# Optimization experiments

Measured on AMD Instinct MI355X. Metric: run time of the kernel, lower is better.

Reference implementation:

```python
import jax, jax.numpy as jnp
import numpy as np

B, S, ENC, DEC = 32, 2048, 1024, 1024
NEG = -1e9


def setup_inputs() -> dict:
    key = jax.random.key(0)
    k1, k2, k3, k4, k5, k6 = jax.random.split(key, 6)
    scale = lambda d: 1.0 / np.sqrt(d)
    return {
        "enc_outputs": jax.random.normal(k1, (B, S, ENC), jnp.float32),
        "dec_hidden": jax.random.normal(k2, (B, DEC), jnp.float32),
        "mask": jax.random.randint(k3, (B, S), 0, 2, jnp.int32),
        "W": jax.random.normal(k4, (ENC, DEC), jnp.float32) * scale(ENC),
        "U": jax.random.normal(k5, (DEC, DEC), jnp.float32) * scale(DEC),
        "v": jax.random.normal(k6, (DEC,), jnp.float32) * scale(DEC),
    }


def reference(enc_outputs, dec_hidden, mask, W, U, v):
    # scores: [B,S] = tanh(enc W + dec U) . v
    proj = jnp.tanh(jnp.einsum('bse,ed->bsd', enc_outputs, W)
                    + jnp.einsum('be,ed->bd', dec_hidden, U)[:, None, :])
    scores = jnp.einsum('bsd,d->bs', proj, v)
    scores = jnp.where(mask == 0, NEG, scores)
    attn = jax.nn.softmax(scores, axis=-1)
    context = jnp.einsum('bs,bse->be', attn, enc_outputs)
    return context, attn
```

## Files before the change

### kernel.cpp

```cpp
#include <hip/hip_runtime.h>
#include <hip/hip_bf16.h>
#include <stdint.h>

#define B_    32
#define S_    2048
#define ENC_  1024
#define DEC_  1024
#define M_    (B_*S_)

typedef __attribute__((ext_vector_type(8))) short bf16x8;
typedef __attribute__((ext_vector_type(4))) float f32x4;

__device__ __forceinline__ unsigned short f2bf(float f) {
  unsigned u = __builtin_bit_cast(unsigned, f);
  u += 0x7FFFu + ((u >> 16) & 1u);
  return (unsigned short)(u >> 16);
}
__device__ __forceinline__ float bf2f(unsigned short u) {
  unsigned x = ((unsigned)u) << 16;
  return __builtin_bit_cast(float, x);
}
__device__ __forceinline__ void async_copy16(void* lds_dst, const void* g_src) {
  __builtin_amdgcn_global_load_lds(
      (const __attribute__((address_space(1))) void*)g_src,
      (__attribute__((address_space(3))) void*)lds_dst, 16, 0, 0);
}
__device__ __forceinline__ float tanh_fast(float x) {
  return 1.f - 2.f / (__expf(2.f * x) + 1.f);
}

__global__ __launch_bounds__(256) void prep_kernel(
    const float* __restrict__ enc, unsigned short* __restrict__ enc16,
    const float* __restrict__ W, const float* __restrict__ dec,
    const float* __restrict__ U, unsigned short* __restrict__ Wt,
    float* __restrict__ t_buf, float* __restrict__ scoresZ,
    float* __restrict__ ctxZ) {
  __shared__ float smem[32 * 33];
  const int blk = blockIdx.x, tid = threadIdx.x;
  if (blk < 8192) {
    const float4* in = (const float4*)enc;
    ushort4* out = (ushort4*)enc16;
    #pragma unroll
    for (int i = 0; i < 8; ++i) {
      int idx = blk * 2048 + i * 256 + tid;
      float4 f = in[idx];
      ushort4 o;
      o.x = f2bf(f.x); o.y = f2bf(f.y); o.z = f2bf(f.z); o.w = f2bf(f.w);
      out[idx] = o;
    }
  } else if (blk < 9216) {
    const int q = blk - 8192;
    const int e0 = (q & 31) * 32, d0 = (q >> 5) * 32;
    const int tx = tid & 31, ty = tid >> 5;
    #pragma unroll
    for (int i = 0; i < 4; ++i)
      smem[(ty + i*8)*33 + tx] = W[(size_t)(e0 + ty + i*8) * DEC_ + d0 + tx];
    __syncthreads();
    #pragma unroll
    for (int i = 0; i < 4; ++i)
      Wt[(size_t)(d0 + ty + i*8) * ENC_ + e0 + tx] = f2bf(smem[tx*33 + ty + i*8]);
  } else if (blk < 9472) {
    const int q = blk - 9216;
    const int dblk = q & 7, b = q >> 3;
    const int d = dblk * 128 + (tid & 127);
    const int h = tid >> 7;
    float acc = 0.f;
    const float* dv = dec + b * DEC_ + h * 512;
    const float* Uc = U + (size_t)(h * 512) * DEC_ + d;
    for (int e = 0; e < 512; ++e) acc += dv[e] * Uc[(size_t)e * DEC_];
    smem[tid] = acc;
    __syncthreads();
    if (tid < 128) t_buf[b * DEC_ + d] = smem[tid] + smem[tid + 128];
  } else {
    const int q = blk - 9472;
    float4 z = {0.f, 0.f, 0.f, 0.f};
    for (int i = tid; i < 512; i += 256) ((float4*)scoresZ)[q * 512 + i] = z;
    for (int i = tid; i < 256; i += 256) ((float4*)ctxZ)[q * 256 + i] = z;
  }
}


#define WT_L  asm volatile("s_waitcnt lgkmcnt(0)" ::: "memory")
#define WT_V4 asm volatile("s_waitcnt vmcnt(4) lgkmcnt(0)" ::: "memory")
#define WT_V0 asm volatile("s_waitcnt vmcnt(0) lgkmcnt(0)" ::: "memory")

#define PHASE(CBUF, Q, KK, BLOAD, TAILWAIT, ...) do {                       \
    bf16x8 af_[4];                                                          \
    const int aA_ = (KK ? aAddr1 : aAddr0) + (CBUF)*32768 + (Q)*16384;      \
    _Pragma("unroll")                                                       \
    for (int mi = 0; mi < 4; ++mi)                                          \
      af_[mi] = *(const bf16x8*)(lds + aA_ + mi*2048);                      \
    if (BLOAD) {                                                            \
      const int bA_ = (KK ? bAddr1 : bAddr0) + (CBUF)*32768;                \
      _Pragma("unroll")                                                     \
      for (int ni = 0; ni < 4; ++ni)                                        \
        bfr[KK][ni] = *(const bf16x8*)(lds + bA_ + ni*2048);                \
    }                                                                       \
    __VA_ARGS__;                                                            \
    __builtin_amdgcn_s_barrier();                                           \
    __builtin_amdgcn_sched_barrier(0);                                      \
    __builtin_amdgcn_s_setprio(1);                                          \
    _Pragma("unroll")                                                       \
    for (int mi = 0; mi < 4; ++mi) {                                        \
      _Pragma("unroll")                                                     \
      for (int ni = 0; ni < 4; ++ni)                                        \
        acc[(Q)*4+mi][ni] = __builtin_amdgcn_mfma_f32_16x16x32_bf16(        \
            af_[mi], bfr[KK][ni], acc[(Q)*4+mi][ni], 0, 0, 0);              \
    }                                                                       \
    __builtin_amdgcn_s_setprio(0);                                          \
    __builtin_amdgcn_sched_barrier(0);                                      \
    TAILWAIT;                                                               \
    __builtin_amdgcn_s_barrier();                                           \
  } while (0)

__global__ __launch_bounds__(512, 2) void scores_kernel(
    const unsigned short* __restrict__ A,
    const unsigned short* __restrict__ Bt,
    const float* __restrict__ tb,
    const float* __restrict__ v,
    float* __restrict__ scores)
{
  extern __shared__ char lds[];

  const int tid  = threadIdx.x;
  const int lane = tid & 63;
  const int wid  = tid >> 6;
  const int wr = wid >> 2, wc = wid & 3;
  const int fr = lane & 15, fq = lane >> 4;

  const int bid = blockIdx.x;
  const int logical = (bid & 7) * 128 + (bid >> 3);
  const int m_blk = logical >> 2, n_blk = logical & 3;
  const int m0 = m_blk << 8;
  const int n0 = n_blk << 8;
  const int b  = m_blk >> 3;

  const int srow   = tid >> 3;
  const int kchunk = (((tid & 7) ^ (srow & 7)) << 3);
  const unsigned short* aP0 = A  + (size_t)(m0       + srow) * ENC_ + kchunk;
  const unsigned short* aP1 = A  + (size_t)(m0 + 64  + srow) * ENC_ + kchunk;
  const unsigned short* aP2 = A  + (size_t)(m0 + 128 + srow) * ENC_ + kchunk;
  const unsigned short* aP3 = A  + (size_t)(m0 + 192 + srow) * ENC_ + kchunk;
  const unsigned short* bP0 = Bt + (size_t)(n0       + srow) * ENC_ + kchunk;
  const unsigned short* bP1 = Bt + (size_t)(n0 + 64  + srow) * ENC_ + kchunk;
  const unsigned short* bP2 = Bt + (size_t)(n0 + 128 + srow) * ENC_ + kchunk;
  const unsigned short* bP3 = Bt + (size_t)(n0 + 192 + srow) * ENC_ + kchunk;
  const int wbase = wid * 1024;

  auto stA = [&](int c, int r, const unsigned short* p) {
    async_copy16(lds + c * 32768 + r * 8192 + wbase, p);
  };
  auto stB = [&](int c, int r, const unsigned short* p) {
    async_copy16(lds + 65536 + c * 32768 + r * 8192 + wbase, p);
  };

  const int sl0 = ((fq)     ^ (fr & 7)) << 4;
  const int sl1 = ((4 + fq) ^ (fr & 7)) << 4;
  const int aAddr0 = (wr * 64 + fr) * 128 + sl0;
  const int aAddr1 = (wr * 64 + fr) * 128 + sl1;
  const int bAddr0 = 65536 + (wc * 64 + fr) * 128 + sl0;
  const int bAddr1 = 65536 + (wc * 64 + fr) * 128 + sl1;

  f32x4 acc[8][4] = {};
  bf16x8 bfr[2][4];

  stA(0, 0, aP0); stA(0, 1, aP1); stA(0, 2, aP2); stA(0, 3, aP3);
  stB(0, 0, bP0); stB(0, 1, bP1); stB(0, 2, bP2); stB(0, 3, bP3);
  stA(1, 0, aP0 + 64); stA(1, 1, aP1 + 64);
  stB(1, 0, bP0 + 64); stB(1, 1, bP1 + 64);
  asm volatile("s_waitcnt vmcnt(4)" ::: "memory");
  __builtin_amdgcn_s_barrier();

  #pragma unroll 1
  for (int J = 0; J < 7; ++J) {
    const int ke = J * 128;
    PHASE(0,0,0,true,  WT_L,  { stB(1,2,bP2+ke+64);  stB(1,3,bP3+ke+64);  });
    PHASE(0,0,1,true,  WT_L,  { stA(1,2,aP2+ke+64);  stA(1,3,aP3+ke+64);  });
    PHASE(0,1,0,false, WT_L,  { stA(0,0,aP0+ke+128); stA(0,1,aP1+ke+128); });
    PHASE(0,1,1,false, WT_V4, { stB(0,0,bP0+ke+128); stB(0,1,bP1+ke+128); });
    PHASE(1,0,0,true,  WT_L,  { stB(0,2,bP2+ke+128); stB(0,3,bP3+ke+128); });
    PHASE(1,0,1,true,  WT_L,  { stA(0,2,aP2+ke+128); stA(0,3,aP3+ke+128); });
    PHASE(1,1,0,false, WT_L,  { stA(1,0,aP0+ke+192); stA(1,1,aP1+ke+192); });
    PHASE(1,1,1,false, WT_V4, { stB(1,0,bP0+ke+192); stB(1,1,bP1+ke+192); });
  }
  {
    const int ke = 896;
    PHASE(0,0,0,true,  WT_L,  { stB(1,2,bP2+ke+64); stB(1,3,bP3+ke+64); });
    PHASE(0,0,1,true,  WT_L,  { stA(1,2,aP2+ke+64); stA(1,3,aP3+ke+64); });
    PHASE(0,1,0,false, WT_L,  {});
    PHASE(0,1,1,false, WT_V0, {});
    PHASE(1,0,0,true,  WT_L,  {});
    PHASE(1,0,1,true,  WT_L,  {});
    PHASE(1,1,0,false, WT_L,  {});
    PHASE(1,1,1,false, WT_V0, {});
  }

  asm volatile("s_waitcnt vmcnt(0) lgkmcnt(0)" ::: "memory");
  __builtin_amdgcn_s_barrier();
  float* sloc = (float*)lds;
  if (tid < 256) sloc[tid] = 0.f;
  __syncthreads();

  float vv[4], tv[4];
  #pragma unroll
  for (int ni = 0; ni < 4; ++ni) {
    int col = n0 + wc * 64 + ni * 16 + fr;
    vv[ni] = v[col];
    tv[ni] = tb[b * DEC_ + col];
  }
  #pragma unroll
  for (int mi = 0; mi < 8; ++mi) {
    #pragma unroll
    for (int j = 0; j < 4; ++j) {
      float p = 0.f;
      #pragma unroll
      for (int ni = 0; ni < 4; ++ni)
        p += vv[ni] * tanh_fast(acc[mi][ni][j] + tv[ni]);
      p += __shfl_xor(p, 1);
      p += __shfl_xor(p, 2);
      p += __shfl_xor(p, 4);
      p += __shfl_xor(p, 8);
      if (fr == 0)
        atomicAdd(&sloc[(mi >> 2) * 128 + wr * 64 + (mi & 3) * 16 + fq * 4 + j], p);
    }
  }
  __syncthreads();
  if (tid < 256) atomicAdd(&scores[m0 + tid], sloc[tid]);
}

__global__ __launch_bounds__(256) void softmax_kernel(
    const float* __restrict__ scores, const int* __restrict__ mask,
    float* __restrict__ attn) {
  const int b = blockIdx.x;
  const int tid = threadIdx.x;
  const int lane = tid & 63, w = tid >> 6;
  __shared__ float wred[4];
  float loc[8];
  float mx = -3.0e38f;
  #pragma unroll
  for (int i = 0; i < 8; ++i) {
    int s = tid + i * 256;
    float val = (mask[b * S_ + s] == 0) ? -1e9f : scores[b * S_ + s];
    loc[i] = val;
    mx = fmaxf(mx, val);
  }
  #pragma unroll
  for (int m = 1; m < 64; m <<= 1) mx = fmaxf(mx, __shfl_xor(mx, m));
  if (lane == 0) wred[w] = mx;
  __syncthreads();
  mx = fmaxf(fmaxf(wred[0], wred[1]), fmaxf(wred[2], wred[3]));
  __syncthreads();
  float sum = 0.f;
  #pragma unroll
  for (int i = 0; i < 8; ++i) { loc[i] = __expf(loc[i] - mx); sum += loc[i]; }
  #pragma unroll
  for (int m = 1; m < 64; m <<= 1) sum += __shfl_xor(sum, m);
  if (lane == 0) wred[w] = sum;
  __syncthreads();
  float inv = 1.f / (wred[0] + wred[1] + wred[2] + wred[3]);
  #pragma unroll
  for (int i = 0; i < 8; ++i) attn[b * S_ + tid + i * 256] = loc[i] * inv;
}

__global__ __launch_bounds__(256) void ctx_kernel(
    const unsigned short* __restrict__ enc16,
    const float* __restrict__ attn,
    float* __restrict__ ctx) {
  const int b  = blockIdx.x;
  const int s0 = blockIdx.y * 256;
  const int tid = threadIdx.x;
  const ushort4* base = reinterpret_cast<const ushort4*>(
      enc16 + ((size_t)b * S_ + s0) * ENC_) + tid;
  float a0 = 0.f, a1 = 0.f, a2 = 0.f, a3 = 0.f;
  for (int s = 0; s < 256; ++s) {
    float a = attn[b * S_ + s0 + s];
    ushort4 ev = base[(size_t)s * 256];
    a0 += a * bf2f(ev.x); a1 += a * bf2f(ev.y);
    a2 += a * bf2f(ev.z); a3 += a * bf2f(ev.w);
  }
  float* c = ctx + (size_t)b * ENC_ + tid * 4;
  atomicAdd(c + 0, a0); atomicAdd(c + 1, a1);
  atomicAdd(c + 2, a2); atomicAdd(c + 3, a3);
}

extern "C" void kernel_launch(void* const* d_in, const int* in_sizes, int n_in,
                              void* d_out, int out_size, void* d_ws, size_t ws_size,
                              hipStream_t stream) {
  const float* enc  = (const float*)d_in[0];
  const float* dec  = (const float*)d_in[1];
  const int*   mask = (const int*)  d_in[2];
  const float* W    = (const float*)d_in[3];
  const float* U    = (const float*)d_in[4];
  const float* v    = (const float*)d_in[5];

  float* out  = (float*)d_out;
  float* ctx  = out;
  float* attn = out + B_ * ENC_;

  char* ws = (char*)d_ws;
  unsigned short* enc16 = (unsigned short*)ws;
  unsigned short* Wt    = (unsigned short*)(ws + (size_t)M_ * ENC_ * 2);
  float* t_buf  = (float*)(ws + (size_t)M_ * ENC_ * 2 + (size_t)ENC_ * DEC_ * 2);
  float* scores = (float*)((char*)t_buf + (size_t)B_ * DEC_ * 4);

  (void)hipFuncSetAttribute((const void*)scores_kernel,
                            hipFuncAttributeMaxDynamicSharedMemorySize, 131072);

  prep_kernel<<<9504, 256, 0, stream>>>(enc, enc16, W, dec, U, Wt,
                                        t_buf, scores, ctx);

  scores_kernel<<<1024, 512, 131072, stream>>>(enc16, Wt, t_buf, v, scores);

  softmax_kernel<<<B_, 256, 0, stream>>>(scores, mask, attn);

  ctx_kernel<<<dim3(B_, S_ / 256), 256, 0, stream>>>(enc16, attn, ctx);
}
```

Before: 258.1 us.

## Fuse softmax into context kernel and reorder prep blocks with wider enc conversion

New measurement: 249.0 us. 1.04x faster.

```diff
diff --git a/kernel.cpp b/kernel.cpp
--- a/kernel.cpp
+++ b/kernel.cpp
@@ -10,6 +10,7 @@
 
 typedef __attribute__((ext_vector_type(8))) short bf16x8;
 typedef __attribute__((ext_vector_type(4))) float f32x4;
+typedef __attribute__((ext_vector_type(8))) unsigned short u16x8;
 
 __device__ __forceinline__ unsigned short f2bf(float f) {
   unsigned u = __builtin_bit_cast(unsigned, f);
@@ -37,20 +38,8 @@
     float* __restrict__ ctxZ) {
   __shared__ float smem[32 * 33];
   const int blk = blockIdx.x, tid = threadIdx.x;
-  if (blk < 8192) {
-    const float4* in = (const float4*)enc;
-    ushort4* out = (ushort4*)enc16;
-    #pragma unroll
-    for (int i = 0; i < 8; ++i) {
-      int idx = blk * 2048 + i * 256 + tid;
-      float4 f = in[idx];
-      ushort4 o;
-      o.x = f2bf(f.x); o.y = f2bf(f.y); o.z = f2bf(f.z); o.w = f2bf(f.w);
-      out[idx] = o;
-    }
-  } else if (blk < 9216) {
-    const int q = blk - 8192;
-    const int e0 = (q & 31) * 32, d0 = (q >> 5) * 32;
+  if (blk < 1024) {
+    const int e0 = (blk & 31) * 32, d0 = (blk >> 5) * 32;
     const int tx = tid & 31, ty = tid >> 5;
     #pragma unroll
     for (int i = 0; i < 4; ++i)
@@ -59,8 +48,8 @@
     #pragma unroll
     for (int i = 0; i < 4; ++i)
       Wt[(size_t)(d0 + ty + i*8) * ENC_ + e0 + tx] = f2bf(smem[tx*33 + ty + i*8]);
-  } else if (blk < 9472) {
-    const int q = blk - 9216;
+  } else if (blk < 1280) {
+    const int q = blk - 1024;
     const int dblk = q & 7, b = q >> 3;
     const int d = dblk * 128 + (tid & 127);
     const int h = tid >> 7;
@@ -71,11 +60,24 @@
     smem[tid] = acc;
     __syncthreads();
     if (tid < 128) t_buf[b * DEC_ + d] = smem[tid] + smem[tid + 128];
-  } else {
-    const int q = blk - 9472;
+  } else if (blk < 1312) {
+    const int q = blk - 1280;
     float4 z = {0.f, 0.f, 0.f, 0.f};
     for (int i = tid; i < 512; i += 256) ((float4*)scoresZ)[q * 512 + i] = z;
     for (int i = tid; i < 256; i += 256) ((float4*)ctxZ)[q * 256 + i] = z;
+  } else {
+    const int q = blk - 1312;
+    const float4* in = (const float4*)enc;
+    u16x8* out = (u16x8*)enc16;
+    #pragma unroll
+    for (int i = 0; i < 4; ++i) {
+      int u = q * 1024 + i * 256 + tid;
+      float4 f0 = in[2*u], f1 = in[2*u + 1];
+      u16x8 o;
+      o[0] = f2bf(f0.x); o[1] = f2bf(f0.y); o[2] = f2bf(f0.z); o[3] = f2bf(f0.w);
+      o[4] = f2bf(f1.x); o[5] = f2bf(f1.y); o[6] = f2bf(f1.z); o[7] = f2bf(f1.w);
+      out[u] = o;
+    }
   }
 }
 
@@ -228,12 +230,14 @@
   if (tid < 256) atomicAdd(&scores[m0 + tid], sloc[tid]);
 }
 
-__global__ __launch_bounds__(256) void softmax_kernel(
+__global__ __launch_bounds__(256) void sm_ctx_kernel(
     const float* __restrict__ scores, const int* __restrict__ mask,
-    float* __restrict__ attn) {
-  const int b = blockIdx.x;
+    const unsigned short* __restrict__ enc16,
+    float* __restrict__ attn, float* __restrict__ ctx) {
+  const int b = blockIdx.x, y = blockIdx.y;
   const int tid = threadIdx.x;
   const int lane = tid & 63, w = tid >> 6;
+  __shared__ float att[S_];
   __shared__ float wred[4];
   float loc[8];
   float mx = -3.0e38f;
@@ -259,21 +263,20 @@
   __syncthreads();
   float inv = 1.f / (wred[0] + wred[1] + wred[2] + wred[3]);
   #pragma unroll
-  for (int i = 0; i < 8; ++i) attn[b * S_ + tid + i * 256] = loc[i] * inv;
-}
-
-__global__ __launch_bounds__(256) void ctx_kernel(
-    const unsigned short* __restrict__ enc16,
-    const float* __restrict__ attn,
-    float* __restrict__ ctx) {
-  const int b  = blockIdx.x;
-  const int s0 = blockIdx.y * 256;
-  const int tid = threadIdx.x;
+  for (int i = 0; i < 8; ++i) {
+    float a = loc[i] * inv;
+    att[tid + i * 256] = a;
+    if (y == 0) attn[b * S_ + tid + i * 256] = a;
+  }
+  __syncthreads();
+
+  const int s0 = y * 128;
   const ushort4* base = reinterpret_cast<const ushort4*>(
       enc16 + ((size_t)b * S_ + s0) * ENC_) + tid;
   float a0 = 0.f, a1 = 0.f, a2 = 0.f, a3 = 0.f;
-  for (int s = 0; s < 256; ++s) {
-    float a = attn[b * S_ + s0 + s];
+  #pragma unroll 4
+  for (int s = 0; s < 128; ++s) {
+    float a = att[s0 + s];
     ushort4 ev = base[(size_t)s * 256];
     a0 += a * bf2f(ev.x); a1 += a * bf2f(ev.y);
     a2 += a * bf2f(ev.z); a3 += a * bf2f(ev.w);
@@ -311,7 +314,5 @@
 
   scores_kernel<<<1024, 512, 131072, stream>>>(enc16, Wt, t_buf, v, scores);
 
-  softmax_kernel<<<B_, 256, 0, stream>>>(scores, mask, attn);
-
-  ctx_kernel<<<dim3(B_, S_ / 256), 256, 0, stream>>>(enc16, attn, ctx);
-}
+  sm_ctx_kernel<<<dim3(B_, 16), 256, 0, stream>>>(scores, mask, enc16, attn, ctx);
+}
```
